# Kernel optimization log

Hardware: AMD Instinct MI355X
Metric: run time of the kernel (lower is better)

The kernel has to match this reference:

```python
import jax, jax.numpy as jnp
import numpy as np

SIZE = 1024
D = 65536


def setup_inputs() -> dict:
    key = jax.random.key(0)
    k_x, k_w, k_b, k_a, k_m = jax.random.split(key, 5)
    x = jax.random.normal(k_x, (SIZE,), dtype=jnp.float32)
    # Projection_2 weight: final init is normal_(0, 1) (normalization in reset_parameters is overwritten)
    weight = jax.random.normal(k_w, (D, SIZE), dtype=jnp.float32)
    # bias ~ Uniform(0, 2*pi), shape (d, size)
    bias = jax.random.uniform(k_b, (D, SIZE), dtype=jnp.float32, minval=0.0, maxval=2.0 * np.pi)
    # alpha[ts] ~ Uniform(0, 1), shape (1, size)
    alpha = jax.random.uniform(k_a, (1, SIZE), dtype=jnp.float32)
    # M is model state (zeros at init, updated online); use random state for a meaningful baseline
    M = jax.random.normal(k_m, (D,), dtype=jnp.float32)
    return {"x": x, "weight": weight, "bias": bias, "alpha": alpha, "M": M, "ts": 0}


def reference(x, weight, bias, alpha, M, ts):
    # ts selects alpha[ts]; alpha is passed directly here.
    # Projection: (1, size) * (d, size) broadcast -> (d, size)
    proj = x[None, :] * weight
    # Nonlinear encode: cos(proj + bias) * sin(proj)
    enc = jnp.cos(proj + bias) * jnp.sin(proj)            # (d, size)
    enc2 = enc * alpha                                     # (d, size)
    # multiset(transpose(enc2)): sum over the size axis -> (d,)
    bundled = enc2.sum(axis=1)
    # hard_quantize: sign to {-1, +1}
    q = jnp.where(bundled > 0, 1.0, -1.0).astype(jnp.float32)  # (d,)
    hvs = enc.T                                            # (size, d)
    # model_result = F.linear(q, M) -> scalar dot product
    model_result = jnp.dot(q, M)
    return (model_result, q, hvs)
```

## Files before the change

kernel.cpp:

```cpp
#include <hip/hip_runtime.h>

#define SIZE_N 1024
#define DDIM   65536
#define D_TILE 64
#define S_CHUNK 64
#define NCHUNK (SIZE_N / S_CHUNK)
#define PITCH  65

__device__ __forceinline__ float sin2pi(float r) {
    return __builtin_amdgcn_sinf(__builtin_amdgcn_fractf(r));
}
__device__ __forceinline__ float cos2pi(float r) {
    return __builtin_amdgcn_cosf(__builtin_amdgcn_fractf(r));
}

#define INV2PI 0.15915494309189535f

__global__ __launch_bounds__(256, 4) void reghd_main(
    const float* __restrict__ x,
    const float* __restrict__ w,
    const float* __restrict__ bias,
    const float* __restrict__ alpha,
    const float* __restrict__ M,
    float* __restrict__ out)
{
    __shared__ float tile[S_CHUNK * PITCH];

    const int t      = threadIdx.x;
    const int lane16 = t & 15;
    const int grp    = t >> 4;
    const int d0     = blockIdx.x * D_TILE;

    float* __restrict__ hvs = out + 1 + DDIM;

    float acc[4] = {0.f, 0.f, 0.f, 0.f};

    for (int c = 0; c < NCHUNK; ++c) {
        const int s0 = c * S_CHUNK;
        const int sx = lane16 * 4;

        const float4 x4 = *reinterpret_cast<const float4*>(x + s0 + sx);
        const float4 a4 = *reinterpret_cast<const float4*>(alpha + s0 + sx);

        const float xr0 = x4.x * INV2PI;
        const float xr1 = x4.y * INV2PI;
        const float xr2 = x4.z * INV2PI;
        const float xr3 = x4.w * INV2PI;

        #pragma unroll
        for (int p = 0; p < 4; ++p) {
            const int row = grp + 16 * p;
            const size_t base = (size_t)(d0 + row) * SIZE_N + s0 + sx;
            const float4 w4 = *reinterpret_cast<const float4*>(w + base);
            const float4 b4 = *reinterpret_cast<const float4*>(bias + base);

            const float r0 = xr0 * w4.x;
            const float r1 = xr1 * w4.y;
            const float r2 = xr2 * w4.z;
            const float r3 = xr3 * w4.w;
            const float rb0 = fmaf(b4.x, INV2PI, r0);
            const float rb1 = fmaf(b4.y, INV2PI, r1);
            const float rb2 = fmaf(b4.z, INV2PI, r2);
            const float rb3 = fmaf(b4.w, INV2PI, r3);

            const float e0 = cos2pi(rb0) * sin2pi(r0);
            const float e1 = cos2pi(rb1) * sin2pi(r1);
            const float e2 = cos2pi(rb2) * sin2pi(r2);
            const float e3 = cos2pi(rb3) * sin2pi(r3);

            tile[(sx + 0) * PITCH + row] = e0;
            tile[(sx + 1) * PITCH + row] = e1;
            tile[(sx + 2) * PITCH + row] = e2;
            tile[(sx + 3) * PITCH + row] = e3;

            acc[p] += e0 * a4.x + e1 * a4.y + e2 * a4.z + e3 * a4.w;
        }
        __syncthreads();

        #pragma unroll
        for (int p2 = 0; p2 < 16; ++p2) {
            const int idx  = t + 256 * p2;
            const int srow = idx >> 6;
            const int dl   = idx & 63;
            const float v  = tile[srow * PITCH + dl];
            hvs[(size_t)(s0 + srow) * DDIM + d0 + dl] = v;
        }
        __syncthreads();
    }

    float local_dot = 0.f;
    #pragma unroll
    for (int p = 0; p < 4; ++p) {
        float s = acc[p];
        #pragma unroll
        for (int m = 1; m < 16; m <<= 1) s += __shfl_xor(s, m);
        if (lane16 == 0) {
            const int d = d0 + grp + 16 * p;
            const float qv = (s > 0.f) ? 1.f : -1.f;
            out[1 + d] = qv;
            local_dot += qv * M[d];
        }
    }
    local_dot += __shfl_xor(local_dot, 16);
    local_dot += __shfl_xor(local_dot, 32);
    if ((t & 63) == 0) atomicAdd(out, local_dot);
}

extern "C" void kernel_launch(void* const* d_in, const int* in_sizes, int n_in,
                              void* d_out, int out_size, void* d_ws, size_t ws_size,
                              hipStream_t stream) {
    const float* x     = (const float*)d_in[0];
    const float* w     = (const float*)d_in[1];
    const float* bias  = (const float*)d_in[2];
    const float* alpha = (const float*)d_in[3];
    const float* M     = (const float*)d_in[4];
    float* out = (float*)d_out;

    hipMemsetAsync(out, 0, sizeof(float), stream);

    reghd_main<<<dim3(DDIM / D_TILE), dim3(256), 0, stream>>>(x, w, bias, alpha, M, out);
}
```

Baseline: 725.8 us.

## Halve D tile, double-buffer LDS, prefetch next chunk, nontemporal hvs stores

```diff
diff --git a/kernel.cpp b/kernel.cpp
--- a/kernel.cpp
+++ b/kernel.cpp
@@ -2,10 +2,12 @@
 
 #define SIZE_N 1024
 #define DDIM   65536
-#define D_TILE 64
+#define D_TILE 32
 #define S_CHUNK 64
 #define NCHUNK (SIZE_N / S_CHUNK)
-#define PITCH  65
+#define PITCH  (D_TILE + 1)
+
+#define INV2PI 0.15915494309189535f
 
 __device__ __forceinline__ float sin2pi(float r) {
     return __builtin_amdgcn_sinf(__builtin_amdgcn_fractf(r));
@@ -14,9 +16,7 @@
     return __builtin_amdgcn_cosf(__builtin_amdgcn_fractf(r));
 }
 
-#define INV2PI 0.15915494309189535f
-
-__global__ __launch_bounds__(256, 4) void reghd_main(
+__global__ __launch_bounds__(256, 8) void reghd_main(
     const float* __restrict__ x,
     const float* __restrict__ w,
     const float* __restrict__ bias,
@@ -24,78 +24,100 @@
     const float* __restrict__ M,
     float* __restrict__ out)
 {
-    __shared__ float tile[S_CHUNK * PITCH];
+    __shared__ float tile[2][S_CHUNK * PITCH];
 
     const int t      = threadIdx.x;
     const int lane16 = t & 15;
     const int grp    = t >> 4;
     const int d0     = blockIdx.x * D_TILE;
+    const int sx     = lane16 * 4;
+
+    const int srow0 = t >> 5;
+    const int dl    = t & 31;
 
     float* __restrict__ hvs = out + 1 + DDIM;
 
-    float acc[4] = {0.f, 0.f, 0.f, 0.f};
+    float acc0 = 0.f, acc1 = 0.f;
 
+    float4 w4a = *reinterpret_cast<const float4*>(w    + (size_t)(d0 + grp)      * SIZE_N + sx);
+    float4 b4a = *reinterpret_cast<const float4*>(bias + (size_t)(d0 + grp)      * SIZE_N + sx);
+    float4 w4b = *reinterpret_cast<const float4*>(w    + (size_t)(d0 + grp + 16) * SIZE_N + sx);
+    float4 b4b = *reinterpret_cast<const float4*>(bias + (size_t)(d0 + grp + 16) * SIZE_N + sx);
+
+    #pragma unroll 2
     for (int c = 0; c < NCHUNK; ++c) {
         const int s0 = c * S_CHUNK;
-        const int sx = lane16 * 4;
+        float* __restrict__ buf = tile[c & 1];
 
         const float4 x4 = *reinterpret_cast<const float4*>(x + s0 + sx);
         const float4 a4 = *reinterpret_cast<const float4*>(alpha + s0 + sx);
-
         const float xr0 = x4.x * INV2PI;
         const float xr1 = x4.y * INV2PI;
         const float xr2 = x4.z * INV2PI;
         const float xr3 = x4.w * INV2PI;
 
-        #pragma unroll
-        for (int p = 0; p < 4; ++p) {
-            const int row = grp + 16 * p;
-            const size_t base = (size_t)(d0 + row) * SIZE_N + s0 + sx;
-            const float4 w4 = *reinterpret_cast<const float4*>(w + base);
-            const float4 b4 = *reinterpret_cast<const float4*>(bias + base);
+        {
+            const float r0 = xr0 * w4a.x, r1 = xr1 * w4a.y, r2 = xr2 * w4a.z, r3 = xr3 * w4a.w;
+            const float e0 = cos2pi(fmaf(b4a.x, INV2PI, r0)) * sin2pi(r0);
+            const float e1 = cos2pi(fmaf(b4a.y, INV2PI, r1)) * sin2pi(r1);
+            const float e2 = cos2pi(fmaf(b4a.z, INV2PI, r2)) * sin2pi(r2);
+            const float e3 = cos2pi(fmaf(b4a.w, INV2PI, r3)) * sin2pi(r3);
+            buf[(sx + 0) * PITCH + grp] = e0;
+            buf[(sx + 1) * PITCH + grp] = e1;
+            buf[(sx + 2) * PITCH + grp] = e2;
+            buf[(sx + 3) * PITCH + grp] = e3;
+            acc0 += e0 * a4.x + e1 * a4.y + e2 * a4.z + e3 * a4.w;
+        }
+        {
+            const float r0 = xr0 * w4b.x, r1 = xr1 * w4b.y, r2 = xr2 * w4b.z, r3 = xr3 * w4b.w;
+            const float e0 = cos2pi(fmaf(b4b.x, INV2PI, r0)) * sin2pi(r0);
+            const float e1 = cos2pi(fmaf(b4b.y, INV2PI, r1)) * sin2pi(r1);
+            const float e2 = cos2pi(fmaf(b4b.z, INV2PI, r2)) * sin2pi(r2);
+            const float e3 = cos2pi(fmaf(b4b.w, INV2PI, r3)) * sin2pi(r3);
+            buf[(sx + 0) * PITCH + grp + 16] = e0;
+            buf[(sx + 1) * PITCH + grp + 16] = e1;
+            buf[(sx + 2) * PITCH + grp + 16] = e2;
+            buf[(sx + 3) * PITCH + grp + 16] = e3;
+            acc1 += e0 * a4.x + e1 * a4.y + e2 * a4.z + e3 * a4.w;
+        }
 
-            const float r0 = xr0 * w4.x;
-            const float r1 = xr1 * w4.y;
-            const float r2 = xr2 * w4.z;
-            const float r3 = xr3 * w4.w;
-            const float rb0 = fmaf(b4.x, INV2PI, r0);
-            const float rb1 = fmaf(b4.y, INV2PI, r1);
-            const float rb2 = fmaf(b4.z, INV2PI, r2);
-            const float rb3 = fmaf(b4.w, INV2PI, r3);
+        const int s1 = (c + 1 < NCHUNK) ? (s0 + S_CHUNK) : s0;
+        w4a = *reinterpret_cast<const float4*>(w    + (size_t)(d0 + grp)      * SIZE_N + s1 + sx);
+        b4a = *reinterpret_cast<const float4*>(bias + (size_t)(d0 + grp)      * SIZE_N + s1 + sx);
+        w4b = *reinterpret_cast<const float4*>(w    + (size_t)(d0 + grp + 16) * SIZE_N + s1 + sx);
+        b4b = *reinterpret_cast<const float4*>(bias + (size_t)(d0 + grp + 16) * SIZE_N + s1 + sx);
 
-            const float e0 = cos2pi(rb0) * sin2pi(r0);
-            const float e1 = cos2pi(rb1) * sin2pi(r1);
-            const float e2 = cos2pi(rb2) * sin2pi(r2);
-            const float e3 = cos2pi(rb3) * sin2pi(r3);
+        asm volatile("s_waitcnt lgkmcnt(0)\n\ts_barrier" ::: "memory");
 
-            tile[(sx + 0) * PITCH + row] = e0;
-            tile[(sx + 1) * PITCH + row] = e1;
-            tile[(sx + 2) * PITCH + row] = e2;
-            tile[(sx + 3) * PITCH + row] = e3;
-
-            acc[p] += e0 * a4.x + e1 * a4.y + e2 * a4.z + e3 * a4.w;
+        {
+            const float* lsrc = buf + srow0 * PITCH + dl;
+            float*       gdst = hvs + (size_t)(s0 + srow0) * DDIM + d0 + dl;
+            #pragma unroll
+            for (int p2 = 0; p2 < 8; ++p2) {
+                __builtin_nontemporal_store(lsrc[p2 * 8 * PITCH], gdst);
+                gdst += (size_t)8 * DDIM;
+            }
         }
-        __syncthreads();
-
-        #pragma unroll
-        for (int p2 = 0; p2 < 16; ++p2) {
-            const int idx  = t + 256 * p2;
-            const int srow = idx >> 6;
-            const int dl   = idx & 63;
-            const float v  = tile[srow * PITCH + dl];
-            hvs[(size_t)(s0 + srow) * DDIM + d0 + dl] = v;
-        }
-        __syncthreads();
     }
 
     float local_dot = 0.f;
-    #pragma unroll
-    for (int p = 0; p < 4; ++p) {
-        float s = acc[p];
+    {
+        float s = acc0;
         #pragma unroll
         for (int m = 1; m < 16; m <<= 1) s += __shfl_xor(s, m);
         if (lane16 == 0) {
-            const int d = d0 + grp + 16 * p;
+            const int d = d0 + grp;
+            const float qv = (s > 0.f) ? 1.f : -1.f;
+            out[1 + d] = qv;
+            local_dot += qv * M[d];
+        }
+    }
+    {
+        float s = acc1;
+        #pragma unroll
+        for (int m = 1; m < 16; m <<= 1) s += __shfl_xor(s, m);
+        if (lane16 == 0) {
+            const int d = d0 + grp + 16;
             const float qv = (s > 0.f) ? 1.f : -1.f;
             out[1 + d] = qv;
             local_dot += qv * M[d];
```

After: 800.4 us. 10.3% more time.
